# Optimization experiments

Hardware: AMD Instinct MI355X
Metric: run time of the kernel (lower is better)

The kernel has to match this reference:

```python
import jax, jax.numpy as jnp
import numpy as np
from jax import lax

H = 8       # heads == channel dim for conv projections
D = 64      # base_dim (per-head width)
B = 8
N = 1024
EPS = 1e-5  # BatchNorm eps (torch default)


def _bn2d(y, g, b, m, v):
    # inference-mode BatchNorm2d over channel axis 1
    inv = g / jnp.sqrt(v + EPS)
    return (y - m[None, :, None, None]) * inv[None, :, None, None] + b[None, :, None, None]


def _sepconv(xh, dw, dwb, g, bb, m, v, pw, pwb):
    # xh: [b, H, n, d] treated as NCHW; depthwise 3x3 (groups=H) + BN + pointwise 1x1
    y = lax.conv_general_dilated(xh, dw, window_strides=(1, 1),
                                 padding=((1, 1), (1, 1)),
                                 feature_group_count=H,
                                 dimension_numbers=('NCHW', 'OIHW', 'NCHW'))
    y = y + dwb[None, :, None, None]
    y = _bn2d(y, g, bb, m, v)
    # pointwise 1x1 conv == channel mix
    y = jnp.einsum('oc,bchw->bohw', pw[:, :, 0, 0], y) + pwb[None, :, None, None]
    return y


def setup_inputs() -> dict:
    key = jax.random.key(0)
    ks = jax.random.split(key, 12)
    s = 0.1
    x = jax.random.normal(ks[0], (B, N, H * D), jnp.float32)
    dw_w = jax.random.normal(ks[1], (3, H, 1, 3, 3), jnp.float32) * s
    dw_b = jax.random.normal(ks[2], (3, H), jnp.float32) * s
    bn_g = 1.0 + 0.1 * jax.random.normal(ks[3], (3, H), jnp.float32)
    bn_b = jax.random.normal(ks[4], (3, H), jnp.float32) * s
    bn_m = jnp.zeros((3, H), jnp.float32)
    bn_v = jnp.ones((3, H), jnp.float32)
    pw_w = jax.random.normal(ks[5], (3, H, H, 1, 1), jnp.float32) * s
    pw_b = jax.random.normal(ks[6], (3, H), jnp.float32) * s
    re_w = jax.random.normal(ks[7], (H, H, 1, 1), jnp.float32) * 0.3
    re_b = jax.random.normal(ks[8], (H,), jnp.float32) * s
    vn_g = 1.0 + 0.1 * jax.random.normal(ks[9], (H,), jnp.float32)
    vn_b = jax.random.normal(ks[10], (H,), jnp.float32) * s
    vn_m = jnp.zeros((H,), jnp.float32)
    vn_v = jnp.ones((H,), jnp.float32)
    out_w = jax.random.normal(ks[11], (H * D, H * D), jnp.float32) * 0.02
    out_b = jnp.zeros((H * D,), jnp.float32)
    return {"x": x, "dw_w": dw_w, "dw_b": dw_b, "bn_g": bn_g, "bn_b": bn_b,
            "bn_m": bn_m, "bn_v": bn_v, "pw_w": pw_w, "pw_b": pw_b,
            "re_w": re_w, "re_b": re_b, "vn_g": vn_g, "vn_b": vn_b,
            "vn_m": vn_m, "vn_v": vn_v, "out_w": out_w, "out_b": out_b}


def reference(x, dw_w, dw_b, bn_g, bn_b, bn_m, bn_v, pw_w, pw_b,
              re_w, re_b, vn_g, vn_b, vn_m, vn_v, out_w, out_b):
    b, n, hd = x.shape
    d = hd // H
    xh = x.reshape(b, n, H, d).transpose(0, 2, 1, 3)  # [b, h, n, d]
    q, k, v = [
        _sepconv(xh, dw_w[i], dw_b[i], bn_g[i], bn_b[i], bn_m[i], bn_v[i],
                 pw_w[i], pw_b[i])
        for i in range(3)
    ]
    scale = H ** -0.5  # note: original uses dim=heads for scale
    dots = jnp.einsum('bhid,bhjd->bhij', q, k) * scale  # [b,h,n,n]
    attn = jax.nn.softmax(dots, axis=-1)
    # re-attention: 1x1 cross-head conv + BatchNorm (reatten_scale = 1.0)
    attn = jnp.einsum('oc,bcij->boij', re_w[:, :, 0, 0], attn) + re_b[None, :, None, None]
    attn = _bn2d(attn, vn_g, vn_b, vn_m, vn_v)
    out = jnp.einsum('bhij,bhjd->bhid', attn, v)
    out = out.transpose(0, 2, 1, 3).reshape(b, n, hd)
    return out @ out_w.T + out_b
```

## Files before the change

kernel.cpp:

```cpp
#include <hip/hip_runtime.h>


#define EPS 1e-5f
#define SCALE 0.35355339059327373f

typedef float f32x4 __attribute__((ext_vector_type(4)));
typedef short short8 __attribute__((ext_vector_type(8)));

#define MFMA16(a, b, c) __builtin_amdgcn_mfma_f32_16x16x32_bf16(a, b, c, 0, 0, 0)

__device__ __forceinline__ unsigned short f2bf(float f) {
  union { float f; unsigned u; } v; v.f = f;
  return (unsigned short)((v.u + 0x7FFFu + ((v.u >> 16) & 1u)) >> 16);
}
__device__ __forceinline__ float bf2f(unsigned short h) {
  union { unsigned u; float f; } v; v.u = ((unsigned)h) << 16;
  return v.f;
}

__global__ __launch_bounds__(256) void kprep(
    const float* __restrict__ dwb, const float* __restrict__ bng,
    const float* __restrict__ bnb, const float* __restrict__ bnm,
    const float* __restrict__ bnv, const float* __restrict__ pww,
    const float* __restrict__ pwb, const float* __restrict__ rew,
    const float* __restrict__ reb, const float* __restrict__ vng,
    const float* __restrict__ vnb, const float* __restrict__ vnm,
    const float* __restrict__ vnv, const float* __restrict__ outw,
    float* __restrict__ smalls, unsigned short* __restrict__ wh,
    unsigned short* __restrict__ wl) {
  int g = blockIdx.x * 256 + threadIdx.x;
  if (g < 262144) {
    float v = outw[g];
    unsigned short hi = f2bf(v);
    wh[g] = hi;
    wl[g] = f2bf(v - bf2f(hi));
  }
  if (blockIdx.x == 0) {
    int t = threadIdx.x;
    if (t < 64) {
      int o = t >> 3, c = t & 7;
      float s = vng[o] * rsqrtf(vnv[o] + EPS);
      smalls[t] = rew[o * 8 + c] * s;
    }
    if (t < 8) {
      float s = vng[t] * rsqrtf(vnv[t] + EPS);
      smalls[64 + t] = (reb[t] - vnm[t]) * s + vnb[t];
    }
    if (t < 192) {
      int p = t >> 6, rem = t & 63, o = rem >> 3, c = rem & 7;
      float s = bng[p * 8 + c] * rsqrtf(bnv[p * 8 + c] + EPS);
      smalls[72 + t] = pww[(p * 8 + o) * 8 + c] * s;
    }
    if (t < 24) {
      int p = t / 8, o = t & 7;
      float acc = pwb[p * 8 + o];
      for (int c = 0; c < 8; ++c) {
        float s = bng[p * 8 + c] * rsqrtf(bnv[p * 8 + c] + EPS);
        acc += pww[(p * 8 + o) * 8 + c] *
               ((dwb[p * 8 + c] - bnm[p * 8 + c]) * s + bnb[p * 8 + c]);
      }
      smalls[264 + t] = acc;
    }
  }
}

__global__ __launch_bounds__(256) void kqkv(
    const float* __restrict__ x, const float* __restrict__ dww,
    const float* __restrict__ smalls,
    unsigned short* __restrict__ qb, unsigned short* __restrict__ kb,
    float* __restrict__ vf) {
  int t = threadIdx.x;
  int blk = blockIdx.x;
  int b = blk >> 8;
  int n0 = (blk & 255) << 2;
  int d = t & 63;
  int n = n0 + (t >> 6);
  const float* pw_eff = smalls + 72;
  const float* pwb_eff = smalls + 264;
  float y[3][8];
  for (int h = 0; h < 8; ++h) {
    float nb[3][3];
#pragma unroll
    for (int ky = 0; ky < 3; ++ky) {
      int nn = n - 1 + ky;
      bool vr = (nn >= 0) && (nn < 1024);
      const float* xp = x + ((b * 1024 + nn) * 512 + h * 64 + d);
      nb[ky][0] = (vr && d > 0) ? xp[-1] : 0.f;
      nb[ky][1] = vr ? xp[0] : 0.f;
      nb[ky][2] = (vr && d < 63) ? xp[1] : 0.f;
    }
#pragma unroll
    for (int p = 0; p < 3; ++p) {
      const float* w = dww + (p * 8 + h) * 9;
      float a = 0.f;
#pragma unroll
      for (int ky = 0; ky < 3; ++ky)
#pragma unroll
        for (int kx = 0; kx < 3; ++kx) a += w[ky * 3 + kx] * nb[ky][kx];
      y[p][h] = a;
    }
  }
#pragma unroll
  for (int p = 0; p < 3; ++p) {
#pragma unroll
    for (int o = 0; o < 8; ++o) {
      float a = pwb_eff[p * 8 + o];
#pragma unroll
      for (int c = 0; c < 8; ++c) a += pw_eff[p * 64 + o * 8 + c] * y[p][c];
      int idx = ((b * 8 + o) * 1024 + n) * 64 + d;
      if (p == 0) qb[idx] = f2bf(a);
      else if (p == 1) kb[idx] = f2bf(a);
      else vf[idx] = a;
    }
  }
}

__global__ __launch_bounds__(256) void kvsum(const float* __restrict__ vf,
                                             const float* __restrict__ smalls,
                                             float* __restrict__ bvs) {
  int t = blockIdx.x * 256 + threadIdx.x;
  int d = t & 63;
  int h = (t >> 6) & 7;
  int b = t >> 9;
  const float* vp = vf + ((b * 8 + h) * 1024) * 64 + d;
  float s = 0.f;
  for (int n = 0; n < 1024; ++n) s += vp[n * 64];
  bvs[t] = smalls[64 + h] * s;
}

__global__ __launch_bounds__(256) void kvtrans(const float* __restrict__ vf,
                                               unsigned short* __restrict__ vt) {
  __shared__ unsigned short lds[64 * 65];
  int bh = blockIdx.x >> 4;
  int nt = blockIdx.x & 15;
  int t = threadIdx.x;
  const float* src = vf + (bh * 1024 + nt * 64) * 64;
#pragma unroll
  for (int it = 0; it < 16; ++it) {
    int nn = (t >> 6) + it * 4;
    int d = t & 63;
    lds[nn * 65 + d] = f2bf(src[nn * 64 + d]);
  }
  __syncthreads();
  unsigned short* dst = vt + bh * 64 * 1024 + nt * 64;
#pragma unroll
  for (int it = 0; it < 16; ++it) {
    int d = (t >> 6) + it * 4;
    int n = t & 63;
    dst[d * 1024 + n] = lds[n * 65 + d];
  }
}

__global__ __launch_bounds__(512, 2) void kattn(
    const unsigned short* __restrict__ qb, const unsigned short* __restrict__ kb,
    const unsigned short* __restrict__ vt, const float* __restrict__ smalls,
    unsigned short* __restrict__ ohi, unsigned short* __restrict__ olo) {
  __shared__ unsigned short plds[8 * 2048];
  int b = blockIdx.x & 7;
  int it = blockIdx.x >> 3;
  int i0 = it * 32;
  int h = threadIdx.x >> 6;
  int l = threadIdx.x & 63;
  int lrow = l & 15, lgrp = l >> 4;
  const unsigned short* qh = qb + (((b * 8 + h) * 1024) + i0) * 64;
  const unsigned short* kh = kb + ((b * 8 + h) * 1024) * 64;
  const unsigned short* vth = vt + ((b * 8 + h) * 64) * 1024;

  short8 Qf[2][2];
#pragma unroll
  for (int a = 0; a < 2; ++a)
#pragma unroll
    for (int kc = 0; kc < 2; ++kc)
      Qf[a][kc] = *(const short8*)(qh + (a * 16 + lrow) * 64 + kc * 32 + lgrp * 8);

  float Wr[8];
#pragma unroll
  for (int c = 0; c < 8; ++c) Wr[c] = smalls[h * 8 + c];

  float rs[2][4] = {};
  for (int jt = 0; jt < 16; ++jt) {
    short8 Kf[4][2];
#pragma unroll
    for (int q = 0; q < 4; ++q)
#pragma unroll
      for (int kc = 0; kc < 2; ++kc)
        Kf[q][kc] = *(const short8*)(kh + (jt * 64 + q * 16 + lrow) * 64 + kc * 32 + lgrp * 8);
    f32x4 acc[2][4] = {};
#pragma unroll
    for (int kc = 0; kc < 2; ++kc)
#pragma unroll
      for (int a = 0; a < 2; ++a)
#pragma unroll
        for (int q = 0; q < 4; ++q)
          acc[a][q] = MFMA16(Qf[a][kc], Kf[q][kc], acc[a][q]);
#pragma unroll
    for (int a = 0; a < 2; ++a)
#pragma unroll
      for (int q = 0; q < 4; ++q)
#pragma unroll
        for (int r = 0; r < 4; ++r) rs[a][r] += __expf(acc[a][q][r] * SCALE);
  }
#pragma unroll
  for (int a = 0; a < 2; ++a)
#pragma unroll
    for (int r = 0; r < 4; ++r) {
      float v = rs[a][r];
      v += __shfl_xor(v, 1);
      v += __shfl_xor(v, 2);
      v += __shfl_xor(v, 4);
      v += __shfl_xor(v, 8);
      rs[a][r] = 1.f / v;
    }

  f32x4 Oacc[2][4] = {};
  for (int jt = 0; jt < 16; ++jt) {
    short8 Kf[4][2];
#pragma unroll
    for (int q = 0; q < 4; ++q)
#pragma unroll
      for (int kc = 0; kc < 2; ++kc)
        Kf[q][kc] = *(const short8*)(kh + (jt * 64 + q * 16 + lrow) * 64 + kc * 32 + lgrp * 8);
    f32x4 acc[2][4] = {};
#pragma unroll
    for (int kc = 0; kc < 2; ++kc)
#pragma unroll
      for (int a = 0; a < 2; ++a)
#pragma unroll
        for (int q = 0; q < 4; ++q)
          acc[a][q] = MFMA16(Qf[a][kc], Kf[q][kc], acc[a][q]);
#pragma unroll
    for (int a = 0; a < 2; ++a)
#pragma unroll
      for (int r = 0; r < 4; ++r) {
        int i = a * 16 + lgrp * 4 + r;
        int swz = ((i >> 2) & 3) << 4;
        int base = h * 2048 + i * 64;
#pragma unroll
        for (int q = 0; q < 4; ++q) {
          float p = __expf(acc[a][q][r] * SCALE) * rs[a][r];
          plds[base + ((q * 16 + lrow) ^ swz)] = f2bf(p);
        }
      }
    __syncthreads();
    short8 PA[2][2];
#pragma unroll
    for (int a = 0; a < 2; ++a) {
      int irow = a * 16 + lrow;
      int swz = ((irow >> 2) & 3) << 4;
#pragma unroll
      for (int kc = 0; kc < 2; ++kc) {
        int eoff = irow * 64 + ((kc * 32 + lgrp * 8) ^ swz);
        float mixv[8] = {};
#pragma unroll
        for (int c = 0; c < 8; ++c) {
          short8 pv = *(const short8*)&plds[c * 2048 + eoff];
#pragma unroll
          for (int e = 0; e < 8; ++e)
            mixv[e] += Wr[c] * bf2f((unsigned short)pv[e]);
        }
        short8 af;
#pragma unroll
        for (int e = 0; e < 8; ++e) af[e] = (short)f2bf(mixv[e]);
        PA[a][kc] = af;
      }
    }
#pragma unroll
    for (int nq = 0; nq < 4; ++nq)
#pragma unroll
      for (int kc = 0; kc < 2; ++kc) {
        short8 Vf = *(const short8*)(vth + (nq * 16 + lrow) * 1024 + jt * 64 + kc * 32 + lgrp * 8);
#pragma unroll
        for (int a = 0; a < 2; ++a) Oacc[a][nq] = MFMA16(PA[a][kc], Vf, Oacc[a][nq]);
      }
    __syncthreads();
  }
  const float* bvs = smalls + 288;
#pragma unroll
  for (int a = 0; a < 2; ++a)
#pragma unroll
    for (int nq = 0; nq < 4; ++nq)
#pragma unroll
      for (int r = 0; r < 4; ++r) {
        int i = i0 + a * 16 + lgrp * 4 + r;
        int dd = nq * 16 + lrow;
        float o = Oacc[a][nq][r] + bvs[(b * 8 + h) * 64 + dd];
        int idx = ((b * 1024 + i) * 512) + h * 64 + dd;
        unsigned short hi = f2bf(o);
        ohi[idx] = hi;
        olo[idx] = f2bf(o - bf2f(hi));
      }
}

__global__ __launch_bounds__(256) void kout(
    const unsigned short* __restrict__ ohi, const unsigned short* __restrict__ olo,
    const unsigned short* __restrict__ wh, const unsigned short* __restrict__ wl,
    const float* __restrict__ outb, float* __restrict__ out) {
  int w = threadIdx.x >> 6, l = threadIdx.x & 63;
  int lrow = l & 15, lgrp = l >> 4;
  int i0 = blockIdx.x * 128 + w * 32;
  int n0 = blockIdx.y * 64;
  f32x4 acc[2][4] = {};
  for (int kc = 0; kc < 16; ++kc) {
    short8 Ah[2], Al[2], Bh[4], Bl[4];
#pragma unroll
    for (int a = 0; a < 2; ++a) {
      int ro = (i0 + a * 16 + lrow) * 512 + kc * 32 + lgrp * 8;
      Ah[a] = *(const short8*)(ohi + ro);
      Al[a] = *(const short8*)(olo + ro);
    }
#pragma unroll
    for (int nq = 0; nq < 4; ++nq) {
      int ro = (n0 + nq * 16 + lrow) * 512 + kc * 32 + lgrp * 8;
      Bh[nq] = *(const short8*)(wh + ro);
      Bl[nq] = *(const short8*)(wl + ro);
    }
#pragma unroll
    for (int a = 0; a < 2; ++a)
#pragma unroll
      for (int nq = 0; nq < 4; ++nq) {
        acc[a][nq] = MFMA16(Ah[a], Bh[nq], acc[a][nq]);
        acc[a][nq] = MFMA16(Ah[a], Bl[nq], acc[a][nq]);
        acc[a][nq] = MFMA16(Al[a], Bh[nq], acc[a][nq]);
      }
  }
#pragma unroll
  for (int a = 0; a < 2; ++a)
#pragma unroll
    for (int nq = 0; nq < 4; ++nq)
#pragma unroll
      for (int r = 0; r < 4; ++r) {
        int row = i0 + a * 16 + lgrp * 4 + r;
        int n = n0 + nq * 16 + lrow;
        out[row * 512 + n] = acc[a][nq][r] + outb[n];
      }
}

extern "C" void kernel_launch(void* const* d_in, const int* in_sizes, int n_in,
                              void* d_out, int out_size, void* d_ws, size_t ws_size,
                              hipStream_t stream) {
  const float* x   = (const float*)d_in[0];
  const float* dww = (const float*)d_in[1];
  const float* dwb = (const float*)d_in[2];
  const float* bng = (const float*)d_in[3];
  const float* bnb = (const float*)d_in[4];
  const float* bnm = (const float*)d_in[5];
  const float* bnv = (const float*)d_in[6];
  const float* pww = (const float*)d_in[7];
  const float* pwb = (const float*)d_in[8];
  const float* rew = (const float*)d_in[9];
  const float* reb = (const float*)d_in[10];
  const float* vng = (const float*)d_in[11];
  const float* vnb = (const float*)d_in[12];
  const float* vnm = (const float*)d_in[13];
  const float* vnv = (const float*)d_in[14];
  const float* outw = (const float*)d_in[15];
  const float* outb = (const float*)d_in[16];

  char* ws = (char*)d_ws;
  const size_t MB = 1024 * 1024;
  unsigned short* qb  = (unsigned short*)(ws);
  unsigned short* kb  = (unsigned short*)(ws + 8 * MB);
  unsigned short* vt  = (unsigned short*)(ws + 16 * MB);
  float*          vf  = (float*)(ws + 24 * MB);
  unsigned short* ohi = (unsigned short*)(ws + 40 * MB);
  unsigned short* olo = (unsigned short*)(ws + 48 * MB);
  unsigned short* wh  = (unsigned short*)(ws + 56 * MB);
  unsigned short* wl  = (unsigned short*)(ws + 56 * MB + 512 * 1024);
  float*       smalls = (float*)(ws + 57 * MB);

  hipLaunchKernelGGL(kprep, dim3(1024), dim3(256), 0, stream,
                     dwb, bng, bnb, bnm, bnv, pww, pwb, rew, reb, vng, vnb,
                     vnm, vnv, outw, smalls, wh, wl);
  hipLaunchKernelGGL(kqkv, dim3(2048), dim3(256), 0, stream,
                     x, dww, smalls, qb, kb, vf);
  hipLaunchKernelGGL(kvsum, dim3(16), dim3(256), 0, stream, vf, smalls, smalls + 288);
  hipLaunchKernelGGL(kvtrans, dim3(1024), dim3(256), 0, stream, vf, vt);
  hipLaunchKernelGGL(kattn, dim3(256), dim3(512), 0, stream,
                     qb, kb, vt, smalls, ohi, olo);
  hipLaunchKernelGGL(kout, dim3(64, 8), dim3(256), 0, stream,
                     ohi, olo, wh, wl, outb, (float*)d_out);
}
```

Before: 326.0 us.

## Restructure attention: 16-row tiles, redistributed cross-head mix, fused V-sum into transpose

The attention kernel now processes 16 query rows per block instead of 32, doubling the grid to 512 blocks and raising the occupancy hint to 4. The cross-head re-attention mix is redistributed so each lane mixes two probability columns across all eight heads, using scalar-broadcast weights held in registers. The mixed results are staged in a second swizzled LDS buffer. The softmax scale is folded into Q at projection time. The separate V column-sum kernel is removed: the transpose kernel accumulates it with atomics into a buffer that the prep kernel zeroes. The aim is better latency hiding and cheaper mixing, at the cost of an extra LDS round-trip with barrier per tile and reloading K/V for half as many rows.

```diff
diff --git a/kernel.cpp b/kernel.cpp
--- a/kernel.cpp
+++ b/kernel.cpp
@@ -6,6 +6,7 @@
 
 typedef float f32x4 __attribute__((ext_vector_type(4)));
 typedef short short8 __attribute__((ext_vector_type(8)));
+typedef unsigned short ushort;
 
 #define MFMA16(a, b, c) __builtin_amdgcn_mfma_f32_16x16x32_bf16(a, b, c, 0, 0, 0)
 
@@ -16,6 +17,11 @@
 __device__ __forceinline__ float bf2f(unsigned short h) {
   union { unsigned u; float f; } v; v.u = ((unsigned)h) << 16;
   return v.f;
+}
+__device__ __forceinline__ int cvtpk(float lo, float hi) {
+  int r;
+  asm("v_cvt_pk_bf16_f32 %0, %1, %2" : "=v"(r) : "v"(lo), "v"(hi));
+  return r;
 }
 
 __global__ __launch_bounds__(256) void kprep(
@@ -26,15 +32,17 @@
     const float* __restrict__ reb, const float* __restrict__ vng,
     const float* __restrict__ vnb, const float* __restrict__ vnm,
     const float* __restrict__ vnv, const float* __restrict__ outw,
-    float* __restrict__ smalls, unsigned short* __restrict__ wh,
-    unsigned short* __restrict__ wl) {
+    float* __restrict__ smalls, float* __restrict__ vsum,
+    ushort* __restrict__ wh, ushort* __restrict__ wl) {
   int g = blockIdx.x * 256 + threadIdx.x;
   if (g < 262144) {
     float v = outw[g];
-    unsigned short hi = f2bf(v);
+    ushort hi = f2bf(v);
     wh[g] = hi;
     wl[g] = f2bf(v - bf2f(hi));
   }
+  if (blockIdx.x >= 1 && blockIdx.x <= 16)
+    vsum[(blockIdx.x - 1) * 256 + threadIdx.x] = 0.f;
   if (blockIdx.x == 0) {
     int t = threadIdx.x;
     if (t < 64) {
@@ -67,7 +75,7 @@
 __global__ __launch_bounds__(256) void kqkv(
     const float* __restrict__ x, const float* __restrict__ dww,
     const float* __restrict__ smalls,
-    unsigned short* __restrict__ qb, unsigned short* __restrict__ kb,
+    ushort* __restrict__ qb, ushort* __restrict__ kb,
     float* __restrict__ vf) {
   int t = threadIdx.x;
   int blk = blockIdx.x;
@@ -108,192 +116,190 @@
 #pragma unroll
       for (int c = 0; c < 8; ++c) a += pw_eff[p * 64 + o * 8 + c] * y[p][c];
       int idx = ((b * 8 + o) * 1024 + n) * 64 + d;
-      if (p == 0) qb[idx] = f2bf(a);
+      if (p == 0) qb[idx] = f2bf(a * SCALE);
       else if (p == 1) kb[idx] = f2bf(a);
       else vf[idx] = a;
     }
   }
 }
 
-__global__ __launch_bounds__(256) void kvsum(const float* __restrict__ vf,
-                                             const float* __restrict__ smalls,
-                                             float* __restrict__ bvs) {
-  int t = blockIdx.x * 256 + threadIdx.x;
-  int d = t & 63;
-  int h = (t >> 6) & 7;
-  int b = t >> 9;
-  const float* vp = vf + ((b * 8 + h) * 1024) * 64 + d;
-  float s = 0.f;
-  for (int n = 0; n < 1024; ++n) s += vp[n * 64];
-  bvs[t] = smalls[64 + h] * s;
-}
-
 __global__ __launch_bounds__(256) void kvtrans(const float* __restrict__ vf,
-                                               unsigned short* __restrict__ vt) {
-  __shared__ unsigned short lds[64 * 65];
+                                               ushort* __restrict__ vt,
+                                               float* __restrict__ vsum) {
+  __shared__ ushort lds[64 * 65];
+  __shared__ float red[256];
   int bh = blockIdx.x >> 4;
   int nt = blockIdx.x & 15;
   int t = threadIdx.x;
   const float* src = vf + (bh * 1024 + nt * 64) * 64;
+  float part = 0.f;
 #pragma unroll
   for (int it = 0; it < 16; ++it) {
     int nn = (t >> 6) + it * 4;
     int d = t & 63;
-    lds[nn * 65 + d] = f2bf(src[nn * 64 + d]);
-  }
+    float v = src[nn * 64 + d];
+    part += v;
+    lds[nn * 65 + d] = f2bf(v);
+  }
+  red[t] = part;
   __syncthreads();
-  unsigned short* dst = vt + bh * 64 * 1024 + nt * 64;
+  ushort* dst = vt + bh * 64 * 1024 + nt * 64;
 #pragma unroll
   for (int it = 0; it < 16; ++it) {
     int d = (t >> 6) + it * 4;
     int n = t & 63;
     dst[d * 1024 + n] = lds[n * 65 + d];
   }
-}
-
-__global__ __launch_bounds__(512, 2) void kattn(
-    const unsigned short* __restrict__ qb, const unsigned short* __restrict__ kb,
-    const unsigned short* __restrict__ vt, const float* __restrict__ smalls,
-    unsigned short* __restrict__ ohi, unsigned short* __restrict__ olo) {
-  __shared__ unsigned short plds[8 * 2048];
+  if (t < 64)
+    atomicAdd(&vsum[bh * 64 + t],
+              red[t] + red[64 + t] + red[128 + t] + red[192 + t]);
+}
+
+__global__ __launch_bounds__(512, 4) void kattn(
+    const ushort* __restrict__ qb, const ushort* __restrict__ kb,
+    const ushort* __restrict__ vt, const float* __restrict__ smalls,
+    const float* __restrict__ vsum,
+    ushort* __restrict__ ohi, ushort* __restrict__ olo) {
+  __shared__ ushort plds[16 * 512];
+  __shared__ ushort mlds[8 * 1024];
   int b = blockIdx.x & 7;
   int it = blockIdx.x >> 3;
-  int i0 = it * 32;
-  int h = threadIdx.x >> 6;
-  int l = threadIdx.x & 63;
+  int i0 = it * 16;
+  int tid = threadIdx.x;
+  int w = tid >> 6;
+  int l = tid & 63;
   int lrow = l & 15, lgrp = l >> 4;
-  const unsigned short* qh = qb + (((b * 8 + h) * 1024) + i0) * 64;
-  const unsigned short* kh = kb + ((b * 8 + h) * 1024) * 64;
-  const unsigned short* vth = vt + ((b * 8 + h) * 64) * 1024;
-
-  short8 Qf[2][2];
-#pragma unroll
-  for (int a = 0; a < 2; ++a)
-#pragma unroll
-    for (int kc = 0; kc < 2; ++kc)
-      Qf[a][kc] = *(const short8*)(qh + (a * 16 + lrow) * 64 + kc * 32 + lgrp * 8);
-
-  float Wr[8];
-#pragma unroll
-  for (int c = 0; c < 8; ++c) Wr[c] = smalls[h * 8 + c];
-
-  float rs[2][4] = {};
+
+  const ushort* qh = qb + ((b * 8 + w) * 1024 + i0) * 64;
+  const ushort* kh = kb + (b * 8 + w) * 1024 * 64;
+  const ushort* vth = vt + (b * 8 + w) * 64 * 1024;
+
+  short8 Qf[2];
+#pragma unroll
+  for (int kc = 0; kc < 2; ++kc)
+    Qf[kc] = *(const short8*)(qh + lrow * 64 + kc * 32 + lgrp * 8);
+
+  int ip = w + ((l >> 5) << 3);
+  int jp = (l & 31) << 1;
+  int s0 = w >> 2;
+  bool s1 = (l >> 5) & 1;
+
+  float Wc[64];
+#pragma unroll
+  for (int z = 0; z < 64; ++z) {
+    int idx = z ^ (s0 << 1);
+    Wc[z] = __builtin_bit_cast(
+        float, __builtin_amdgcn_readfirstlane(
+                   __builtin_bit_cast(int, smalls[idx])));
+  }
+
+  float rs[4] = {0.f, 0.f, 0.f, 0.f};
   for (int jt = 0; jt < 16; ++jt) {
-    short8 Kf[4][2];
+    const ushort* kbase = kh + jt * 64 * 64;
+    f32x4 acc[4] = {};
 #pragma unroll
     for (int q = 0; q < 4; ++q)
 #pragma unroll
-      for (int kc = 0; kc < 2; ++kc)
-        Kf[q][kc] = *(const short8*)(kh + (jt * 64 + q * 16 + lrow) * 64 + kc * 32 + lgrp * 8);
-    f32x4 acc[2][4] = {};
-#pragma unroll
-    for (int kc = 0; kc < 2; ++kc)
-#pragma unroll
-      for (int a = 0; a < 2; ++a)
-#pragma unroll
-        for (int q = 0; q < 4; ++q)
-          acc[a][q] = MFMA16(Qf[a][kc], Kf[q][kc], acc[a][q]);
-#pragma unroll
-    for (int a = 0; a < 2; ++a)
-#pragma unroll
-      for (int q = 0; q < 4; ++q)
-#pragma unroll
-        for (int r = 0; r < 4; ++r) rs[a][r] += __expf(acc[a][q][r] * SCALE);
-  }
-#pragma unroll
-  for (int a = 0; a < 2; ++a)
-#pragma unroll
-    for (int r = 0; r < 4; ++r) {
-      float v = rs[a][r];
-      v += __shfl_xor(v, 1);
-      v += __shfl_xor(v, 2);
-      v += __shfl_xor(v, 4);
-      v += __shfl_xor(v, 8);
-      rs[a][r] = 1.f / v;
-    }
-
-  f32x4 Oacc[2][4] = {};
+      for (int kc = 0; kc < 2; ++kc) {
+        short8 Kf = *(const short8*)(kbase + (q * 16 + lrow) * 64 + kc * 32 + lgrp * 8);
+        acc[q] = MFMA16(Qf[kc], Kf, acc[q]);
+      }
+#pragma unroll
+    for (int q = 0; q < 4; ++q)
+#pragma unroll
+      for (int r = 0; r < 4; ++r) rs[r] += __expf(acc[q][r]);
+  }
+#pragma unroll
+  for (int r = 0; r < 4; ++r) {
+    float v = rs[r];
+    v += __shfl_xor(v, 1);
+    v += __shfl_xor(v, 2);
+    v += __shfl_xor(v, 4);
+    v += __shfl_xor(v, 8);
+    rs[r] = 1.f / v;
+  }
+
+  f32x4 Oacc[4] = {};
   for (int jt = 0; jt < 16; ++jt) {
-    short8 Kf[4][2];
+    const ushort* kbase = kh + jt * 64 * 64;
+    f32x4 acc[4] = {};
 #pragma unroll
     for (int q = 0; q < 4; ++q)
 #pragma unroll
-      for (int kc = 0; kc < 2; ++kc)
-        Kf[q][kc] = *(const short8*)(kh + (jt * 64 + q * 16 + lrow) * 64 + kc * 32 + lgrp * 8);
-    f32x4 acc[2][4] = {};
-#pragma unroll
-    for (int kc = 0; kc < 2; ++kc)
-#pragma unroll
-      for (int a = 0; a < 2; ++a)
-#pragma unroll
-        for (int q = 0; q < 4; ++q)
-          acc[a][q] = MFMA16(Qf[a][kc], Kf[q][kc], acc[a][q]);
-#pragma unroll
-    for (int a = 0; a < 2; ++a)
+      for (int kc = 0; kc < 2; ++kc) {
+        short8 Kf = *(const short8*)(kbase + (q * 16 + lrow) * 64 + kc * 32 + lgrp * 8);
+        acc[q] = MFMA16(Qf[kc], Kf, acc[q]);
+      }
+#pragma unroll
+    for (int q = 0; q < 4; ++q)
 #pragma unroll
       for (int r = 0; r < 4; ++r) {
-        int i = a * 16 + lgrp * 4 + r;
-        int swz = ((i >> 2) & 3) << 4;
-        int base = h * 2048 + i * 64;
-#pragma unroll
-        for (int q = 0; q < 4; ++q) {
-          float p = __expf(acc[a][q][r] * SCALE) * rs[a][r];
-          plds[base + ((q * 16 + lrow) ^ swz)] = f2bf(p);
-        }
+        float p = __expf(acc[q][r]) * rs[r];
+        int pi = (((lgrp * 4 + r) << 9) + ((q * 16 + lrow) << 3) + w) ^ (lgrp << 1);
+        plds[pi] = (ushort)cvtpk(p, p);
       }
     __syncthreads();
-    short8 PA[2][2];
-#pragma unroll
-    for (int a = 0; a < 2; ++a) {
-      int irow = a * 16 + lrow;
-      int swz = ((irow >> 2) & 3) << 4;
-#pragma unroll
-      for (int kc = 0; kc < 2; ++kc) {
-        int eoff = irow * 64 + ((kc * 32 + lgrp * 8) ^ swz);
-        float mixv[8] = {};
-#pragma unroll
-        for (int c = 0; c < 8; ++c) {
-          short8 pv = *(const short8*)&plds[c * 2048 + eoff];
-#pragma unroll
-          for (int e = 0; e < 8; ++e)
-            mixv[e] += Wr[c] * bf2f((unsigned short)pv[e]);
-        }
-        short8 af;
-#pragma unroll
-        for (int e = 0; e < 8; ++e) af[e] = (short)f2bf(mixv[e]);
-        PA[a][kc] = af;
-      }
+    int pbase = (ip << 9) + (jp << 3);
+    int4 r0 = *(const int4*)&plds[pbase];
+    int4 r1 = *(const int4*)&plds[pbase + 8];
+    int e0[4], e1[4];
+    e0[0] = s1 ? r0.z : r0.x;  e0[1] = s1 ? r0.w : r0.y;
+    e0[2] = s1 ? r0.x : r0.z;  e0[3] = s1 ? r0.y : r0.w;
+    e1[0] = s1 ? r1.z : r1.x;  e1[1] = s1 ? r1.w : r1.y;
+    e1[2] = s1 ? r1.x : r1.z;  e1[3] = s1 ? r1.y : r1.w;
+    float o0[8] = {}, o1[8] = {};
+#pragma unroll
+    for (int m = 0; m < 4; ++m) {
+      float p0l = __builtin_bit_cast(float, e0[m] << 16);
+      float p0h = __builtin_bit_cast(float, (unsigned)e0[m] & 0xffff0000u);
+      float p1l = __builtin_bit_cast(float, e1[m] << 16);
+      float p1h = __builtin_bit_cast(float, (unsigned)e1[m] & 0xffff0000u);
+#pragma unroll
+      for (int o = 0; o < 8; ++o) {
+        o0[o] += Wc[o * 8 + 2 * m] * p0l + Wc[o * 8 + 2 * m + 1] * p0h;
+        o1[o] += Wc[o * 8 + 2 * m] * p1l + Wc[o * 8 + 2 * m + 1] * p1h;
+      }
+    }
+#pragma unroll
+    for (int o = 0; o < 8; ++o) {
+      int pk = cvtpk(o0[o], o1[o]);
+      int mi = ((o << 10) + (ip << 6) + jp) ^ ((ip & 7) << 3);
+      *(int*)&mlds[mi] = pk;
+    }
+    __syncthreads();
+    short8 PA[2];
+#pragma unroll
+    for (int kc = 0; kc < 2; ++kc) {
+      int ai = ((w << 10) + (lrow << 6) + kc * 32 + lgrp * 8) ^ ((lrow & 7) << 3);
+      PA[kc] = *(const short8*)&mlds[ai];
     }
 #pragma unroll
     for (int nq = 0; nq < 4; ++nq)
 #pragma unroll
       for (int kc = 0; kc < 2; ++kc) {
         short8 Vf = *(const short8*)(vth + (nq * 16 + lrow) * 1024 + jt * 64 + kc * 32 + lgrp * 8);
-#pragma unroll
-        for (int a = 0; a < 2; ++a) Oacc[a][nq] = MFMA16(PA[a][kc], Vf, Oacc[a][nq]);
-      }
-    __syncthreads();
-  }
-  const float* bvs = smalls + 288;
-#pragma unroll
-  for (int a = 0; a < 2; ++a)
-#pragma unroll
-    for (int nq = 0; nq < 4; ++nq)
-#pragma unroll
-      for (int r = 0; r < 4; ++r) {
-        int i = i0 + a * 16 + lgrp * 4 + r;
-        int dd = nq * 16 + lrow;
-        float o = Oacc[a][nq][r] + bvs[(b * 8 + h) * 64 + dd];
-        int idx = ((b * 1024 + i) * 512) + h * 64 + dd;
-        unsigned short hi = f2bf(o);
-        ohi[idx] = hi;
-        olo[idx] = f2bf(o - bf2f(hi));
-      }
+        Oacc[nq] = MFMA16(PA[kc], Vf, Oacc[nq]);
+      }
+  }
+
+  float beta = smalls[64 + w];
+#pragma unroll
+  for (int nq = 0; nq < 4; ++nq)
+#pragma unroll
+    for (int r = 0; r < 4; ++r) {
+      int i = i0 + lgrp * 4 + r;
+      int dd = nq * 16 + lrow;
+      float o = Oacc[nq][r] + beta * vsum[(b * 8 + w) * 64 + dd];
+      int idx = (b * 1024 + i) * 512 + w * 64 + dd;
+      ushort hi = (ushort)cvtpk(o, o);
+      ohi[idx] = hi;
+      olo[idx] = f2bf(o - bf2f(hi));
+    }
 }
 
 __global__ __launch_bounds__(256) void kout(
-    const unsigned short* __restrict__ ohi, const unsigned short* __restrict__ olo,
-    const unsigned short* __restrict__ wh, const unsigned short* __restrict__ wl,
+    const ushort* __restrict__ ohi, const ushort* __restrict__ olo,
+    const ushort* __restrict__ wh, const ushort* __restrict__ wl,
     const float* __restrict__ outb, float* __restrict__ out) {
   int w = threadIdx.x >> 6, l = threadIdx.x & 63;
   int lrow = l & 15, lgrp = l >> 4;
@@ -358,25 +364,25 @@
 
   char* ws = (char*)d_ws;
   const size_t MB = 1024 * 1024;
-  unsigned short* qb  = (unsigned short*)(ws);
-  unsigned short* kb  = (unsigned short*)(ws + 8 * MB);
-  unsigned short* vt  = (unsigned short*)(ws + 16 * MB);
-  float*          vf  = (float*)(ws + 24 * MB);
-  unsigned short* ohi = (unsigned short*)(ws + 40 * MB);
-  unsigned short* olo = (unsigned short*)(ws + 48 * MB);
-  unsigned short* wh  = (unsigned short*)(ws + 56 * MB);
-  unsigned short* wl  = (unsigned short*)(ws + 56 * MB + 512 * 1024);
-  float*       smalls = (float*)(ws + 57 * MB);
+  ushort* qb  = (ushort*)(ws);
+  ushort* kb  = (ushort*)(ws + 8 * MB);
+  ushort* vt  = (ushort*)(ws + 16 * MB);
+  float*  vf  = (float*)(ws + 24 * MB);
+  ushort* ohi = (ushort*)(ws + 40 * MB);
+  ushort* olo = (ushort*)(ws + 48 * MB);
+  ushort* wh  = (ushort*)(ws + 56 * MB);
+  ushort* wl  = (ushort*)(ws + 56 * MB + 512 * 1024);
+  float* smalls = (float*)(ws + 57 * MB);
+  float* vsum   = (float*)(ws + 57 * MB + 4096);
 
   hipLaunchKernelGGL(kprep, dim3(1024), dim3(256), 0, stream,
                      dwb, bng, bnb, bnm, bnv, pww, pwb, rew, reb, vng, vnb,
-                     vnm, vnv, outw, smalls, wh, wl);
+                     vnm, vnv, outw, smalls, vsum, wh, wl);
   hipLaunchKernelGGL(kqkv, dim3(2048), dim3(256), 0, stream,
                      x, dww, smalls, qb, kb, vf);
-  hipLaunchKernelGGL(kvsum, dim3(16), dim3(256), 0, stream, vf, smalls, smalls + 288);
-  hipLaunchKernelGGL(kvtrans, dim3(1024), dim3(256), 0, stream, vf, vt);
-  hipLaunchKernelGGL(kattn, dim3(256), dim3(512), 0, stream,
-                     qb, kb, vt, smalls, ohi, olo);
+  hipLaunchKernelGGL(kvtrans, dim3(1024), dim3(256), 0, stream, vf, vt, vsum);
+  hipLaunchKernelGGL(kattn, dim3(512), dim3(512), 0, stream,
+                     qb, kb, vt, smalls, vsum, ohi, olo);
   hipLaunchKernelGGL(kout, dim3(64, 8), dim3(256), 0, stream,
                      ohi, olo, wh, wl, outb, (float*)d_out);
 }
```

After: 349.2 us. +7.1%, slower.
